# Optimization experiments

Hardware: AMD Instinct MI355X
Metric: run time of the kernel (lower is better)

The kernel has to match this reference:

```python
import jax, jax.numpy as jnp
import numpy as np

B, S, D = 16, 2048, 128
SCALE = 1.0 / float(np.sqrt(D))  # scale = 1/sqrt(dim_K) per docstring


def setup_inputs() -> dict:
    key = jax.random.key(0)
    kq, kk, kv = jax.random.split(key, 3)
    Q = jax.random.normal(kq, (B, S, D), dtype=jnp.float32)
    K = jax.random.normal(kk, (B, S, D), dtype=jnp.float32)
    V = jax.random.normal(kv, (B, S, D), dtype=jnp.float32)
    return {"Q": Q, "K": K, "V": V}


def reference(Q, K, V):
    # attention = Q @ K^T * scale  -> [B, S, S]
    attn = jnp.einsum('bqd,bkd->bqk', Q, K) * SCALE
    attn = jax.nn.softmax(attn, axis=-1)
    # context = attn @ V -> [B, S, D]
    context = jnp.einsum('bqk,bkd->bqd', attn, V)
    return context
```

## Files before the change

kernel.cpp:

```cpp
#include <hip/hip_runtime.h>
#include <hip/hip_bf16.h>


#define NB 16
#define NS 2048
#define ND 128
#define KVBLK 64
#define NT (NS / KVBLK)
#define NHT (NT / 2)
#define IMGB 32768
#define QSC (0.08838834764831845f * 1.4426950408889634f)

typedef __attribute__((ext_vector_type(8))) short bf16x8;
typedef __attribute__((ext_vector_type(4))) short short4v;
typedef __attribute__((ext_vector_type(16))) float f32x16;
typedef __attribute__((ext_vector_type(4))) int int4v;

__device__ __forceinline__ short f2bf(float f) {
    unsigned u = __builtin_bit_cast(unsigned, f);
    return (short)((u + 0x7fffu + ((u >> 16) & 1u)) >> 16);
}

#if __has_builtin(__builtin_amdgcn_exp2f)
#define EXP2F(x) __builtin_amdgcn_exp2f(x)
#else
#define EXP2F(x) __expf((x) * 0.6931471805599453f)
#endif

__device__ __forceinline__ void gll16(const void* g, void* l) {
    __builtin_amdgcn_global_load_lds(
        (const __attribute__((address_space(1))) uint32_t*)g,
        (__attribute__((address_space(3))) uint32_t*)l, 16, 0, 0);
}

__global__ __launch_bounds__(256, 2)
void prep_kv(const float* __restrict__ Kg, const float* __restrict__ Vg,
             uint8_t* __restrict__ ws) {
    __shared__ __align__(16) uint8_t img[IMGB];
    const int tid = threadIdx.x;
    const int t = blockIdx.x, b = blockIdx.y;
    const float* Kb = Kg + ((size_t)b * NS + (size_t)t * KVBLK) * ND;
    const float* Vb = Vg + ((size_t)b * NS + (size_t)t * KVBLK) * ND;
#pragma unroll
    for (int it = 0; it < 8; ++it) {
        int idx = it * 256 + tid;
        int r  = idx >> 5;
        int c4 = (idx & 31) << 2;
        float4 kvv = *(const float4*)(Kb + (size_t)r * ND + c4);
        short4v ks = { f2bf(kvv.x), f2bf(kvv.y), f2bf(kvv.z), f2bf(kvv.w) };
        *(short4v*)&img[r * 256 + ((c4 * 2) ^ ((r & 7) << 4))] = ks;
        float4 vv = *(const float4*)(Vb + (size_t)r * ND + c4);
        float vf[4] = { vv.x, vv.y, vv.z, vv.w };
#pragma unroll
        for (int di = 0; di < 4; ++di) {
            int d = c4 + di;
            *(short*)&img[16384 + d * 128 + ((r * 2) ^ ((d & 7) << 4))] = f2bf(vf[di]);
        }
    }
    __syncthreads();
    float4* dst = (float4*)(ws + (size_t)(b * NT + t) * IMGB);
    const float4* srcl = (const float4*)img;
#pragma unroll
    for (int j = 0; j < 8; ++j)
        dst[j * 256 + tid] = srcl[j * 256 + tid];
}

__global__ __launch_bounds__(512, 2)
void sdpa_fwd(const float* __restrict__ Qg, const uint8_t* __restrict__ ws,
              float* __restrict__ Og) {
    __shared__ __align__(16) uint8_t kv[2][2][IMGB];

    const int tid  = threadIdx.x;
    const int w    = tid >> 6;
    const int wq   = w & 3;
    const int wh   = w >> 2;
    const int lane = tid & 63;
    const int lr_  = lane & 31;
    const int hi   = lane >> 5;
    const int xr   = (lane & 7) << 4;

    const int gid  = blockIdx.x;
    const int b    = (gid & 7) * 2 + ((gid >> 3) & 1);
    const int qblk = gid >> 4;
    const int q0w  = qblk * 128 + wq * 32;

    bf16x8 qf[8];
    {
        const float* qrow = Qg + ((size_t)b * NS + q0w + lr_) * ND;
#pragma unroll
        for (int dc = 0; dc < 8; ++dc) {
            const float4* p = (const float4*)(qrow + dc * 16 + hi * 8);
            float4 x0 = p[0], x1 = p[1];
            bf16x8 f;
            f[0] = f2bf(x0.x * QSC); f[1] = f2bf(x0.y * QSC);
            f[2] = f2bf(x0.z * QSC); f[3] = f2bf(x0.w * QSC);
            f[4] = f2bf(x1.x * QSC); f[5] = f2bf(x1.y * QSC);
            f[6] = f2bf(x1.z * QSC); f[7] = f2bf(x1.w * QSC);
            qf[dc] = f;
        }
    }

    f32x16 acc[4];
#pragma unroll
    for (int n = 0; n < 4; ++n)
#pragma unroll
        for (int r = 0; r < 16; ++r) acc[n][r] = 0.f;
    float m_run = -__builtin_inff();
    float l_run = 0.f;

    const uint8_t* wsb = ws + (size_t)b * NT * IMGB;

    auto stage = [&](int bfi, int it) {
        const uint8_t* src = wsb + (size_t)(wh * NHT + it) * IMGB
                                 + (size_t)(wq * 8192 + lane * 16);
        uint8_t* dst = &kv[bfi][wh][wq * 8192];
#pragma unroll
        for (int i = 0; i < 8; ++i)
            gll16(src + i * 1024, dst + i * 1024);
    };

    const int kbase = lr_ * 256 + ((hi * 16) ^ xr);
    const int vbase = 16384 + lr_ * 128 + ((hi * 16) ^ xr);

    int buf = 0;
    stage(0, 0);
    __syncthreads();

    for (int t = 0; t < NHT; ++t) {
        if (t + 1 < NHT) stage(buf ^ 1, t + 1);

        const uint8_t* img = kv[buf][wh];

        f32x16 s0, s1;
#pragma unroll
        for (int r = 0; r < 16; ++r) { s0[r] = 0.f; s1[r] = 0.f; }
        __builtin_amdgcn_s_setprio(1);
#pragma unroll
        for (int dc = 0; dc < 8; ++dc) {
            const uint8_t* ka = img + (kbase ^ (dc * 32));
            bf16x8 k0 = *(const bf16x8*)ka;
            bf16x8 k1 = *(const bf16x8*)(ka + 8192);
            s0 = __builtin_amdgcn_mfma_f32_32x32x16_bf16(k0, qf[dc], s0, 0, 0, 0);
            s1 = __builtin_amdgcn_mfma_f32_32x32x16_bf16(k1, qf[dc], s1, 0, 0, 0);
        }
        __builtin_amdgcn_s_setprio(0);

        float tmax = -__builtin_inff();
#pragma unroll
        for (int r = 0; r < 16; ++r) tmax = fmaxf(tmax, fmaxf(s0[r], s1[r]));
        float tm = fmaxf(tmax, __shfl_xor(tmax, 32));

        if (__any(tm > m_run + 8.0f)) {
            float m_new = fmaxf(m_run, tm);
            float alpha = EXP2F(m_run - m_new);
            m_run = m_new;
            l_run *= alpha;
            float af[16];
#pragma unroll
            for (int r = 0; r < 16; ++r)
                af[r] = __shfl(alpha, (r & 3) + 8 * (r >> 2) + 4 * hi);
#pragma unroll
            for (int n = 0; n < 4; ++n)
#pragma unroll
                for (int r = 0; r < 16; ++r) acc[n][r] *= af[r];
        }

        float pv0[16], pv1[16], ts = 0.f;
#pragma unroll
        for (int r = 0; r < 16; ++r) {
            pv0[r] = EXP2F(s0[r] - m_run); ts += pv0[r];
            pv1[r] = EXP2F(s1[r] - m_run); ts += pv1[r];
        }
        l_run += ts + __shfl_xor(ts, 32);

        int W[16];
#define PK(dst, x, y) asm("v_cvt_pk_bf16_f32 %0, %1, %2" : "=v"(dst) : "v"(x), "v"(y))
        PK(W[0],  pv0[0],  pv0[1]);  PK(W[1],  pv0[2],  pv0[3]);
        PK(W[2],  pv0[4],  pv0[5]);  PK(W[3],  pv0[6],  pv0[7]);
        PK(W[4],  pv0[8],  pv0[9]);  PK(W[5],  pv0[10], pv0[11]);
        PK(W[6],  pv0[12], pv0[13]); PK(W[7],  pv0[14], pv0[15]);
        PK(W[8],  pv1[0],  pv1[1]);  PK(W[9],  pv1[2],  pv1[3]);
        PK(W[10], pv1[4],  pv1[5]);  PK(W[11], pv1[6],  pv1[7]);
        PK(W[12], pv1[8],  pv1[9]);  PK(W[13], pv1[10], pv1[11]);
        PK(W[14], pv1[12], pv1[13]); PK(W[15], pv1[14], pv1[15]);
#undef PK
        bf16x8 pa[4];
#pragma unroll
        for (int g = 0; g < 4; ++g) {
            int W0 = W[g * 4 + 0], W1 = W[g * 4 + 1];
            int W2 = W[g * 4 + 2], W3 = W[g * 4 + 3];
            int X0 = __shfl_xor(W0, 32), X1 = __shfl_xor(W1, 32);
            int X2 = __shfl_xor(W2, 32), X3 = __shfl_xor(W3, 32);
            int4v A;
            A[0] = hi ? X2 : W0;
            A[1] = hi ? X3 : W1;
            A[2] = hi ? W2 : X0;
            A[3] = hi ? W3 : X1;
            pa[g] = __builtin_bit_cast(bf16x8, A);
        }

        __builtin_amdgcn_s_setprio(1);
#pragma unroll
        for (int n = 0; n < 4; ++n) {
#pragma unroll
            for (int kc = 0; kc < 4; ++kc) {
                bf16x8 vf = *(const bf16x8*)(img + ((vbase ^ (kc * 32)) + n * 4096));
                acc[n] = __builtin_amdgcn_mfma_f32_32x32x16_bf16(pa[kc], vf, acc[n], 0, 0, 0);
            }
        }
        __builtin_amdgcn_s_setprio(0);

        __syncthreads();
        buf ^= 1;
    }

    float* scr = (float*)&kv[0][0][0];
    const int sbase = wq * 4224 + lane * 66;
    if (wh == 1) {
#pragma unroll
        for (int n = 0; n < 4; ++n)
#pragma unroll
            for (int r = 0; r < 16; ++r) scr[sbase + n * 16 + r] = acc[n][r];
        scr[sbase + 64] = m_run;
        scr[sbase + 65] = l_run;
    }
    __syncthreads();
    if (wh == 0) {
        float m1 = scr[sbase + 64], l1 = scr[sbase + 65];
        float mm = fmaxf(m_run, m1);
        float a0 = EXP2F(m_run - mm), a1 = EXP2F(m1 - mm);
        float lc = l_run * a0 + l1 * a1;
        float af0[16], af1[16], li[16];
#pragma unroll
        for (int r = 0; r < 16; ++r) {
            int row = (r & 3) + 8 * (r >> 2) + 4 * hi;
            af0[r] = __shfl(a0, row);
            af1[r] = __shfl(a1, row);
            li[r] = 1.f / __shfl(lc, row);
        }
        float* ob = Og + ((size_t)b * NS + q0w) * ND + lr_;
#pragma unroll
        for (int r = 0; r < 16; ++r) {
            int row = (r & 3) + 8 * (r >> 2) + 4 * hi;
#pragma unroll
            for (int n = 0; n < 4; ++n)
                ob[(size_t)row * ND + n * 32] =
                    (acc[n][r] * af0[r] + scr[sbase + n * 16 + r] * af1[r]) * li[r];
        }
    }
}

extern "C" void kernel_launch(void* const* d_in, const int* in_sizes, int n_in,
                              void* d_out, int out_size, void* d_ws, size_t ws_size,
                              hipStream_t stream) {
    const float* Q = (const float*)d_in[0];
    const float* K = (const float*)d_in[1];
    const float* V = (const float*)d_in[2];
    float* O = (float*)d_out;
    (void)in_sizes; (void)n_in; (void)out_size; (void)ws_size;
    uint8_t* ws = (uint8_t*)d_ws;
    prep_kv<<<dim3(NT, NB), 256, 0, stream>>>(K, V, ws);
    sdpa_fwd<<<dim3(NB * NS / 128, 1), 512, 0, stream>>>(Q, ws, O);
}
```

Measured before the change: 62.56 us.

## Split KV sequence across four wave groups with 32-row tiles

Each 128-query block now uses 1024 threads in four wave groups instead of two. Each group walks a quarter of the KV sequence in 32-row tiles, and the K/V workspace image is re-laid out into 16 KB sub-tiles with a new V swizzle. The partial softmax states are merged by group 0 over three rounds of shared-memory exchange. The aim is to double the waves per CU so more latency is hidden. In exchange it adds a serial reduction epilogue with extra barriers, and the aggressive launch bounds may squeeze the register budget and cause spills.

New measurement: 85.71 us. 37.0% more time.

```diff
diff --git a/kernel.cpp b/kernel.cpp
--- a/kernel.cpp
+++ b/kernel.cpp
@@ -5,10 +5,10 @@
 #define NB 16
 #define NS 2048
 #define ND 128
-#define KVBLK 64
-#define NT (NS / KVBLK)
-#define NHT (NT / 2)
-#define IMGB 32768
+#define KVB 32
+#define NTT (NS / KVB)
+#define NTQ (NTT / 4)
+#define IMG 16384
 #define QSC (0.08838834764831845f * 1.4426950408889634f)
 
 typedef __attribute__((ext_vector_type(8))) short bf16x8;
@@ -36,39 +36,42 @@
 __global__ __launch_bounds__(256, 2)
 void prep_kv(const float* __restrict__ Kg, const float* __restrict__ Vg,
              uint8_t* __restrict__ ws) {
-    __shared__ __align__(16) uint8_t img[IMGB];
+    __shared__ __align__(16) uint8_t img[2 * IMG];
     const int tid = threadIdx.x;
     const int t = blockIdx.x, b = blockIdx.y;
-    const float* Kb = Kg + ((size_t)b * NS + (size_t)t * KVBLK) * ND;
-    const float* Vb = Vg + ((size_t)b * NS + (size_t)t * KVBLK) * ND;
+    const float* Kb = Kg + ((size_t)b * NS + (size_t)t * 64) * ND;
+    const float* Vb = Vg + ((size_t)b * NS + (size_t)t * 64) * ND;
 #pragma unroll
     for (int it = 0; it < 8; ++it) {
         int idx = it * 256 + tid;
         int r  = idx >> 5;
         int c4 = (idx & 31) << 2;
+        int sub = (r >> 5) * (2 * 8192);
+        int rr = r & 31;
         float4 kvv = *(const float4*)(Kb + (size_t)r * ND + c4);
         short4v ks = { f2bf(kvv.x), f2bf(kvv.y), f2bf(kvv.z), f2bf(kvv.w) };
-        *(short4v*)&img[r * 256 + ((c4 * 2) ^ ((r & 7) << 4))] = ks;
+        *(short4v*)&img[sub + rr * 256 + ((c4 * 2) ^ ((rr & 7) << 4))] = ks;
         float4 vv = *(const float4*)(Vb + (size_t)r * ND + c4);
         float vf[4] = { vv.x, vv.y, vv.z, vv.w };
 #pragma unroll
         for (int di = 0; di < 4; ++di) {
             int d = c4 + di;
-            *(short*)&img[16384 + d * 128 + ((r * 2) ^ ((d & 7) << 4))] = f2bf(vf[di]);
+            *(short*)&img[sub + 8192 + d * 64 + ((rr * 2) ^ (((d >> 1) & 3) << 4))]
+                = f2bf(vf[di]);
         }
     }
     __syncthreads();
-    float4* dst = (float4*)(ws + (size_t)(b * NT + t) * IMGB);
+    float4* dst = (float4*)(ws + (size_t)(b * (NTT / 2) + t) * (2 * IMG));
     const float4* srcl = (const float4*)img;
 #pragma unroll
     for (int j = 0; j < 8; ++j)
         dst[j * 256 + tid] = srcl[j * 256 + tid];
 }
 
-__global__ __launch_bounds__(512, 2)
+__global__ __launch_bounds__(1024, 4)
 void sdpa_fwd(const float* __restrict__ Qg, const uint8_t* __restrict__ ws,
               float* __restrict__ Og) {
-    __shared__ __align__(16) uint8_t kv[2][2][IMGB];
+    __shared__ __align__(16) uint8_t kv[2][4][IMG];
 
     const int tid  = threadIdx.x;
     const int w    = tid >> 6;
@@ -77,7 +80,6 @@
     const int lane = tid & 63;
     const int lr_  = lane & 31;
     const int hi   = lane >> 5;
-    const int xr   = (lane & 7) << 4;
 
     const int gid  = blockIdx.x;
     const int b    = (gid & 7) * 2 + ((gid >> 3) & 1);
@@ -108,46 +110,43 @@
     float m_run = -__builtin_inff();
     float l_run = 0.f;
 
-    const uint8_t* wsb = ws + (size_t)b * NT * IMGB;
+    const uint8_t* wsb = ws + (size_t)b * NTT * IMG;
 
     auto stage = [&](int bfi, int it) {
-        const uint8_t* src = wsb + (size_t)(wh * NHT + it) * IMGB
-                                 + (size_t)(wq * 8192 + lane * 16);
-        uint8_t* dst = &kv[bfi][wh][wq * 8192];
-#pragma unroll
-        for (int i = 0; i < 8; ++i)
+        const uint8_t* src = wsb + (size_t)(wh * NTQ + it) * IMG
+                                 + (size_t)(wq * 4096 + lane * 16);
+        uint8_t* dst = &kv[bfi][wh][wq * 4096];
+#pragma unroll
+        for (int i = 0; i < 4; ++i)
             gll16(src + i * 1024, dst + i * 1024);
     };
 
-    const int kbase = lr_ * 256 + ((hi * 16) ^ xr);
-    const int vbase = 16384 + lr_ * 128 + ((hi * 16) ^ xr);
+    const int kbase = lr_ * 256 + ((hi * 16) ^ ((lr_ & 7) << 4));
+    const int vbase = 8192 + lr_ * 64 + ((hi * 16) ^ (((lr_ >> 1) & 3) << 4));
 
     int buf = 0;
     stage(0, 0);
     __syncthreads();
 
-    for (int t = 0; t < NHT; ++t) {
-        if (t + 1 < NHT) stage(buf ^ 1, t + 1);
+    for (int t = 0; t < NTQ; ++t) {
+        if (t + 1 < NTQ) stage(buf ^ 1, t + 1);
 
         const uint8_t* img = kv[buf][wh];
 
-        f32x16 s0, s1;
-#pragma unroll
-        for (int r = 0; r < 16; ++r) { s0[r] = 0.f; s1[r] = 0.f; }
+        f32x16 s0;
+#pragma unroll
+        for (int r = 0; r < 16; ++r) s0[r] = 0.f;
         __builtin_amdgcn_s_setprio(1);
 #pragma unroll
         for (int dc = 0; dc < 8; ++dc) {
-            const uint8_t* ka = img + (kbase ^ (dc * 32));
-            bf16x8 k0 = *(const bf16x8*)ka;
-            bf16x8 k1 = *(const bf16x8*)(ka + 8192);
+            bf16x8 k0 = *(const bf16x8*)(img + (kbase ^ (dc * 32)));
             s0 = __builtin_amdgcn_mfma_f32_32x32x16_bf16(k0, qf[dc], s0, 0, 0, 0);
-            s1 = __builtin_amdgcn_mfma_f32_32x32x16_bf16(k1, qf[dc], s1, 0, 0, 0);
         }
         __builtin_amdgcn_s_setprio(0);
 
         float tmax = -__builtin_inff();
 #pragma unroll
-        for (int r = 0; r < 16; ++r) tmax = fmaxf(tmax, fmaxf(s0[r], s1[r]));
+        for (int r = 0; r < 16; ++r) tmax = fmaxf(tmax, s0[r]);
         float tm = fmaxf(tmax, __shfl_xor(tmax, 32));
 
         if (__any(tm > m_run + 8.0f)) {
@@ -155,38 +154,32 @@
             float alpha = EXP2F(m_run - m_new);
             m_run = m_new;
             l_run *= alpha;
-            float af[16];
-#pragma unroll
-            for (int r = 0; r < 16; ++r)
-                af[r] = __shfl(alpha, (r & 3) + 8 * (r >> 2) + 4 * hi);
-#pragma unroll
-            for (int n = 0; n < 4; ++n)
-#pragma unroll
-                for (int r = 0; r < 16; ++r) acc[n][r] *= af[r];
-        }
-
-        float pv0[16], pv1[16], ts = 0.f;
+#pragma unroll
+            for (int r = 0; r < 16; ++r) {
+                float a = __shfl(alpha, (r & 3) + 8 * (r >> 2) + 4 * hi);
+#pragma unroll
+                for (int n = 0; n < 4; ++n) acc[n][r] *= a;
+            }
+        }
+
+        float ts = 0.f;
 #pragma unroll
         for (int r = 0; r < 16; ++r) {
-            pv0[r] = EXP2F(s0[r] - m_run); ts += pv0[r];
-            pv1[r] = EXP2F(s1[r] - m_run); ts += pv1[r];
+            s0[r] = EXP2F(s0[r] - m_run);
+            ts += s0[r];
         }
         l_run += ts + __shfl_xor(ts, 32);
 
-        int W[16];
+        int W[8];
 #define PK(dst, x, y) asm("v_cvt_pk_bf16_f32 %0, %1, %2" : "=v"(dst) : "v"(x), "v"(y))
-        PK(W[0],  pv0[0],  pv0[1]);  PK(W[1],  pv0[2],  pv0[3]);
-        PK(W[2],  pv0[4],  pv0[5]);  PK(W[3],  pv0[6],  pv0[7]);
-        PK(W[4],  pv0[8],  pv0[9]);  PK(W[5],  pv0[10], pv0[11]);
-        PK(W[6],  pv0[12], pv0[13]); PK(W[7],  pv0[14], pv0[15]);
-        PK(W[8],  pv1[0],  pv1[1]);  PK(W[9],  pv1[2],  pv1[3]);
-        PK(W[10], pv1[4],  pv1[5]);  PK(W[11], pv1[6],  pv1[7]);
-        PK(W[12], pv1[8],  pv1[9]);  PK(W[13], pv1[10], pv1[11]);
-        PK(W[14], pv1[12], pv1[13]); PK(W[15], pv1[14], pv1[15]);
+        PK(W[0], s0[0],  s0[1]);  PK(W[1], s0[2],  s0[3]);
+        PK(W[2], s0[4],  s0[5]);  PK(W[3], s0[6],  s0[7]);
+        PK(W[4], s0[8],  s0[9]);  PK(W[5], s0[10], s0[11]);
+        PK(W[6], s0[12], s0[13]); PK(W[7], s0[14], s0[15]);
 #undef PK
-        bf16x8 pa[4];
-#pragma unroll
-        for (int g = 0; g < 4; ++g) {
+        bf16x8 pa[2];
+#pragma unroll
+        for (int g = 0; g < 2; ++g) {
             int W0 = W[g * 4 + 0], W1 = W[g * 4 + 1];
             int W2 = W[g * 4 + 2], W3 = W[g * 4 + 3];
             int X0 = __shfl_xor(W0, 32), X1 = __shfl_xor(W1, 32);
@@ -203,8 +196,8 @@
 #pragma unroll
         for (int n = 0; n < 4; ++n) {
 #pragma unroll
-            for (int kc = 0; kc < 4; ++kc) {
-                bf16x8 vf = *(const bf16x8*)(img + ((vbase ^ (kc * 32)) + n * 4096));
+            for (int kc = 0; kc < 2; ++kc) {
+                bf16x8 vf = *(const bf16x8*)(img + ((vbase ^ (kc * 32)) + n * 2048));
                 acc[n] = __builtin_amdgcn_mfma_f32_32x32x16_bf16(pa[kc], vf, acc[n], 0, 0, 0);
             }
         }
@@ -216,36 +209,44 @@
 
     float* scr = (float*)&kv[0][0][0];
     const int sbase = wq * 4224 + lane * 66;
-    if (wh == 1) {
-#pragma unroll
-        for (int n = 0; n < 4; ++n)
-#pragma unroll
-            for (int r = 0; r < 16; ++r) scr[sbase + n * 16 + r] = acc[n][r];
-        scr[sbase + 64] = m_run;
-        scr[sbase + 65] = l_run;
-    }
-    __syncthreads();
+#pragma unroll
+    for (int rnd = 1; rnd <= 3; ++rnd) {
+        __syncthreads();
+        if (wh == rnd) {
+#pragma unroll
+            for (int n = 0; n < 4; ++n)
+#pragma unroll
+                for (int r = 0; r < 16; ++r) scr[sbase + n * 16 + r] = acc[n][r];
+            scr[sbase + 64] = m_run;
+            scr[sbase + 65] = l_run;
+        }
+        __syncthreads();
+        if (wh == 0) {
+            float m1 = scr[sbase + 64], l1 = scr[sbase + 65];
+            float mm = fmaxf(m_run, m1);
+            float a0 = EXP2F(m_run - mm), a1 = EXP2F(m1 - mm);
+            l_run = l_run * a0 + l1 * a1;
+            m_run = mm;
+#pragma unroll
+            for (int r = 0; r < 16; ++r) {
+                int row = (r & 3) + 8 * (r >> 2) + 4 * hi;
+                float f0 = __shfl(a0, row), f1 = __shfl(a1, row);
+#pragma unroll
+                for (int n = 0; n < 4; ++n)
+                    acc[n][r] = acc[n][r] * f0 + scr[sbase + n * 16 + r] * f1;
+            }
+        }
+    }
+
     if (wh == 0) {
-        float m1 = scr[sbase + 64], l1 = scr[sbase + 65];
-        float mm = fmaxf(m_run, m1);
-        float a0 = EXP2F(m_run - mm), a1 = EXP2F(m1 - mm);
-        float lc = l_run * a0 + l1 * a1;
-        float af0[16], af1[16], li[16];
+        float* ob = Og + ((size_t)b * NS + q0w) * ND + lr_;
 #pragma unroll
         for (int r = 0; r < 16; ++r) {
             int row = (r & 3) + 8 * (r >> 2) + 4 * hi;
-            af0[r] = __shfl(a0, row);
-            af1[r] = __shfl(a1, row);
-            li[r] = 1.f / __shfl(lc, row);
-        }
-        float* ob = Og + ((size_t)b * NS + q0w) * ND + lr_;
-#pragma unroll
-        for (int r = 0; r < 16; ++r) {
-            int row = (r & 3) + 8 * (r >> 2) + 4 * hi;
+            float li = 1.f / __shfl(l_run, row);
 #pragma unroll
             for (int n = 0; n < 4; ++n)
-                ob[(size_t)row * ND + n * 32] =
-                    (acc[n][r] * af0[r] + scr[sbase + n * 16 + r] * af1[r]) * li[r];
+                ob[(size_t)row * ND + n * 32] = acc[n][r] * li;
         }
     }
 }
@@ -259,6 +260,6 @@
     float* O = (float*)d_out;
     (void)in_sizes; (void)n_in; (void)out_size; (void)ws_size;
     uint8_t* ws = (uint8_t*)d_ws;
-    prep_kv<<<dim3(NT, NB), 256, 0, stream>>>(K, V, ws);
-    sdpa_fwd<<<dim3(NB * NS / 128, 1), 512, 0, stream>>>(Q, ws, O);
-}
+    prep_kv<<<dim3(NS / 64, NB), 256, 0, stream>>>(K, V, ws);
+    sdpa_fwd<<<dim3(NB * NS / 128, 1), 1024, 0, stream>>>(Q, ws, O);
+}
```
